# Kernel optimization log

Measured on AMD Instinct MI355X. Metric: run time of the kernel, lower is better.

The kernel has to match this reference:

```python
import jax, jax.numpy as jnp
import numpy as np

B, L, C, H, W = 2, 3, 64, 32, 32
DI, N, DT_RANK, K = 128, 16, 4, 4  # d_inner=2*C, d_state, dt_rank=ceil(C/16), 4 scan dirs


def setup_inputs() -> dict:
    key = jax.random.key(0)
    ks = iter(jax.random.split(key, 48))
    nrm = lambda shape, s=0.02: jax.random.normal(next(ks), shape, jnp.float32) * s
    return {
        "image_sequence": jax.random.normal(next(ks), (B, L, C, H, W), jnp.float32),
        "difficult_zone": jax.random.normal(next(ks), (B, C, H, W), jnp.float32),
        "sigma": jax.random.uniform(next(ks), (B, C, H, W), jnp.float32),
        # LayerNorm2d applied to each frame
        "norm_g": jnp.ones((C,)), "norm_b": jnp.zeros((C,)),
        # ConvolutionalResBlock (in=3C -> out=C), GroupNorm(num_groups=1)
        "gn1_g": jnp.ones((3 * C,)), "gn1_b": jnp.zeros((3 * C,)),
        "conv1_w": nrm((C, 3 * C, 3, 3)), "conv1_b": jnp.zeros((C,)),
        "gn2_g": jnp.ones((C,)), "gn2_b": jnp.zeros((C,)),
        "conv2_w": nrm((C, C, 3, 3)), "conv2_b": jnp.zeros((C,)),
        "skip_w": nrm((C, 3 * C, 1, 1)), "skip_b": jnp.zeros((C,)),
        # VSSBlock pre-norms
        "ln1_g": jnp.ones((C,)), "ln1_b": jnp.zeros((C,)),
        "ln2_g": jnp.ones((C,)), "ln2_b": jnp.zeros((C,)),
        # SS2D
        "in_proj_w": nrm((2 * DI, C)),
        "dwconv_w": nrm((DI, 1, 3, 3)), "dwconv_b": jnp.zeros((DI,)),
        "x_proj_w": nrm((K, DT_RANK + 2 * N, DI)),
        "dt_proj_w": nrm((K, DI, DT_RANK), 0.1),
        "dt_proj_b": jnp.log(jnp.expm1(jnp.full((K, DI), 0.01, jnp.float32))),
        "A_logs": jnp.log(jnp.tile(jnp.arange(1, N + 1, dtype=jnp.float32), (K * DI, 1))),
        "Ds": jnp.ones((K * DI,)),
        "out_norm_g": jnp.ones((DI,)), "out_norm_b": jnp.zeros((DI,)),
        "out_proj_w": nrm((C, DI)),
        # Mlp (hidden = C)
        "fc1_w": nrm((C, C)), "fc1_b": jnp.zeros((C,)),
        "fc2_w": nrm((C, C)), "fc2_b": jnp.zeros((C,)),
    }


def _ln(x, g, b, eps=1e-5):  # layernorm over last axis
    m = x.mean(-1, keepdims=True)
    v = x.var(-1, keepdims=True)
    return (x - m) * jax.lax.rsqrt(v + eps) * g + b


def _ln2d(x, g, b, eps=1e-6):  # per-pixel channel layernorm, NCHW
    m = x.mean(1, keepdims=True)
    v = x.var(1, keepdims=True)
    return (x - m) * jax.lax.rsqrt(v + eps) * g[None, :, None, None] + b[None, :, None, None]


def _gn1(x, g, b, eps=1e-5):  # GroupNorm(num_groups=1), NCHW
    m = x.mean((1, 2, 3), keepdims=True)
    v = x.var((1, 2, 3), keepdims=True)
    return (x - m) * jax.lax.rsqrt(v + eps) * g[None, :, None, None] + b[None, :, None, None]


def _conv(x, w, b, pad):
    y = jax.lax.conv_general_dilated(x, w, (1, 1), [(pad, pad), (pad, pad)],
                                     dimension_numbers=("NCHW", "OIHW", "NCHW"))
    return y + b[None, :, None, None]


def _forward(image_sequence, difficult_zone, sigma, norm_g, norm_b, gn1_g, gn1_b,
             conv1_w, conv1_b, gn2_g, gn2_b, conv2_w, conv2_b, skip_w, skip_b,
             ln1_g, ln1_b, ln2_g, ln2_b, in_proj_w, dwconv_w, dwconv_b, x_proj_w,
             dt_proj_w, dt_proj_b, A_logs, Ds, out_norm_g, out_norm_b, out_proj_w,
             fc1_w, fc1_b, fc2_w, fc2_b):
    b, l, c, h, w = image_sequence.shape
    bl, L2 = b * l, h * w
    # fold frame loop into batch (identical math per frame in the torch loop)
    frames = _ln2d(image_sequence.reshape(bl, c, h, w), norm_g, norm_b)
    dz = jnp.broadcast_to(difficult_zone[:, None], (b, l, c, h, w)).reshape(bl, c, h, w)
    sg = jnp.broadcast_to(sigma[:, None], (b, l, c, h, w)).reshape(bl, c, h, w)
    x = jnp.concatenate([dz, frames, sg], axis=1)  # [bl, 3c, h, w]
    # channel compressor: pre-act conv res block
    hdn = _conv(jax.nn.silu(_gn1(x, gn1_g, gn1_b)), conv1_w, conv1_b, 1)
    hdn = _conv(jax.nn.silu(_gn1(hdn, gn2_g, gn2_b)), conv2_w, conv2_b, 1)
    x = hdn + _conv(x, skip_w, skip_b, 0)          # [bl, c, h, w]
    x = x.transpose(0, 2, 3, 1)                    # [bl, h, w, c]
    # --- VSSBlock (pre-norm): x = x + SS2D(LN(x)) ---
    xn = _ln(x, ln1_g, ln1_b)
    xz = xn @ in_proj_w.T                          # [bl,h,w,2*DI]
    xc, z = jnp.split(xz, 2, axis=-1)
    xc = xc.transpose(0, 3, 1, 2)                  # [bl, DI, h, w]
    xc = jax.lax.conv_general_dilated(xc, dwconv_w, (1, 1), [(1, 1), (1, 1)],
                                      dimension_numbers=("NCHW", "OIHW", "NCHW"),
                                      feature_group_count=DI) + dwconv_b[None, :, None, None]
    xc = jax.nn.silu(xc)
    # 4-direction scan inputs (HW, WH, and their reverses)
    xf = xc.reshape(bl, DI, L2)
    xt = xc.transpose(0, 1, 3, 2).reshape(bl, DI, L2)
    xs = jnp.stack([xf, xt], axis=1)
    xs = jnp.concatenate([xs, jnp.flip(xs, axis=-1)], axis=1)  # [bl, 4, DI, L2]
    x_dbl = jnp.einsum("bkdl,kcd->bkcl", xs, x_proj_w)
    dts, Bs, Cs = jnp.split(x_dbl, [DT_RANK, DT_RANK + N], axis=2)
    dts = jnp.einsum("bkrl,kdr->bkdl", dts, dt_proj_w) + dt_proj_b[None, :, :, None]
    dts = jax.nn.softplus(dts)                     # [bl, 4, DI, L2]
    A = -jnp.exp(A_logs).reshape(K, DI, N)
    dA = jnp.exp(dts[..., None] * A[None, :, :, None, :])            # [bl,4,DI,L2,N]
    dBu = dts[..., None] * Bs.transpose(0, 1, 3, 2)[:, :, None] * xs[..., None]
    a_t = dA.transpose(3, 0, 1, 2, 4)              # [L2, bl, 4, DI, N]
    bu_t = dBu.transpose(3, 0, 1, 2, 4)
    c_t = Cs.transpose(3, 0, 1, 2)                 # [L2, bl, 4, N]

    def step(hid, inp):
        a_i, bu_i, c_i = inp
        hid = a_i * hid + bu_i
        return hid, jnp.einsum("bkdn,bkn->bkd", hid, c_i)

    h0 = jnp.zeros((bl, K, DI, N), xs.dtype)
    _, ys = jax.lax.scan(step, h0, (a_t, bu_t, c_t))                 # [L2, bl, 4, DI]
    ys = ys.transpose(1, 2, 3, 0) + xs * Ds.reshape(K, DI)[None, :, :, None]
    inv = jnp.flip(ys[:, 2:4], axis=-1)
    y = (ys[:, 0] + inv[:, 0]
         + ys[:, 1].reshape(bl, DI, w, h).transpose(0, 1, 3, 2).reshape(bl, DI, L2)
         + inv[:, 1].reshape(bl, DI, w, h).transpose(0, 1, 3, 2).reshape(bl, DI, L2))
    y = _ln(y.transpose(0, 2, 1), out_norm_g, out_norm_b).reshape(bl, h, w, DI)
    y = y * jax.nn.silu(z)
    x = x + y @ out_proj_w.T
    # --- x = x + Mlp(LN(x)) ---
    xn = _ln(x, ln2_g, ln2_b)
    x = x + (jax.nn.gelu(xn @ fc1_w.T + fc1_b, approximate=False) @ fc2_w.T + fc2_b)
    return x.transpose(0, 3, 1, 2).reshape(b, l, c, h, w)


def reference(image_sequence, difficult_zone, sigma, norm_g, norm_b, gn1_g, gn1_b,
              conv1_w, conv1_b, gn2_g, gn2_b, conv2_w, conv2_b, skip_w, skip_b,
              ln1_g, ln1_b, ln2_g, ln2_b, in_proj_w, dwconv_w, dwconv_b, x_proj_w,
              dt_proj_w, dt_proj_b, A_logs, Ds, out_norm_g, out_norm_b, out_proj_w,
              fc1_w, fc1_b, fc2_w, fc2_b):
    return _forward(image_sequence, difficult_zone, sigma, norm_g, norm_b, gn1_g, gn1_b,
                    conv1_w, conv1_b, gn2_g, gn2_b, conv2_w, conv2_b, skip_w, skip_b,
                    ln1_g, ln1_b, ln2_g, ln2_b, in_proj_w, dwconv_w, dwconv_b, x_proj_w,
                    dt_proj_w, dt_proj_b, A_logs, Ds, out_norm_g, out_norm_b, out_proj_w,
                    fc1_w, fc1_b, fc2_w, fc2_b)
```

## Files before the change

### kernel.cpp

```cpp
#include <hip/hip_runtime.h>
#include <math.h>

#define BL    6
#define CCH   64
#define C3    192
#define L2    1024
#define DIC   128
#define NST   16
#define K4    4
#define PSTR  1088
#define NCH   32

#define LOG2E 1.44269504088896340736f
#define LN2C  0.69314718055994530942f

__device__ __forceinline__ float fexp(float x){ return __builtin_amdgcn_exp2f(x*LOG2E); }
__device__ __forceinline__ float fsilu(float x){ return x / (1.f + fexp(-x)); }
__device__ __forceinline__ float fsoftplus(float x){
  if (x > 20.f) return x;
  return __builtin_amdgcn_logf(1.f + fexp(x)) * LN2C;
}
__device__ __forceinline__ float fgelu(float x){
  return 0.5f*x*(1.f + erff(x*0.70710678118654752440f));
}

__global__ __launch_bounds__(256) void k_ln2d(const float* __restrict__ img,
    const float* __restrict__ dz, const float* __restrict__ sg,
    const float* __restrict__ g, const float* __restrict__ b, float* __restrict__ x3c,
    float* __restrict__ psum1, float* __restrict__ psq1){
  __shared__ float ps[4][16], pq[4][16], gs[4], gq[4];
  int s = blockIdx.x >> 6;
  int pg = blockIdx.x & 63;
  int tid = threadIdx.x;
  int px = tid & 15; int cg = tid >> 4;
  int wv = tid >> 6; int lane = tid & 63;
  int p = pg*16 + px;
  int bsmp = s/3;
  const float* fr = img + (size_t)s*CCH*L2;
  float vals[4]; float sm=0.f, sq=0.f;
  #pragma unroll
  for (int j=0;j<4;++j){
    int c = cg*4 + j;
    float v = fr[c*L2 + p];
    vals[j]=v; sm+=v; sq+=v*v;
  }
  sm += __shfl_xor(sm,16,64); sq += __shfl_xor(sq,16,64);
  sm += __shfl_xor(sm,32,64); sq += __shfl_xor(sq,32,64);
  if (lane < 16){ ps[wv][lane]=sm; pq[wv][lane]=sq; }
  __syncthreads();
  sm = ps[0][px]+ps[1][px]+ps[2][px]+ps[3][px];
  sq = pq[0][px]+pq[1][px]+pq[2][px]+pq[3][px];
  float mean = sm*(1.f/CCH); float var = sq*(1.f/CCH)-mean*mean;
  float rs = rsqrtf(var + 1e-6f);
  float* o = x3c + (size_t)s*C3*L2;
  const float* dzp = dz + (size_t)bsmp*CCH*L2;
  const float* sgp = sg + (size_t)bsmp*CCH*L2;
  float gsm=0.f, gsq=0.f;
  #pragma unroll
  for (int j=0;j<4;++j){
    int c = cg*4+j;
    float dzv = dzp[c*L2+p];
    float nv  = (vals[j]-mean)*rs*g[c] + b[c];
    float sgv = sgp[c*L2+p];
    o[c*L2+p] = dzv;
    o[(CCH+c)*L2+p] = nv;
    o[(2*CCH+c)*L2+p] = sgv;
    gsm += dzv+nv+sgv; gsq += dzv*dzv+nv*nv+sgv*sgv;
  }
  for (int m=1;m<64;m<<=1){ gsm+=__shfl_xor(gsm,m,64); gsq+=__shfl_xor(gsq,m,64); }
  if (lane==0){ gs[wv]=gsm; gq[wv]=gsq; }
  __syncthreads();
  if (tid==0){
    psum1[blockIdx.x] = gs[0]+gs[1]+gs[2]+gs[3];
    psq1 [blockIdx.x] = gq[0]+gq[1]+gq[2]+gq[3];
  }
}

__global__ __launch_bounds__(256) void k_gnact_pad(const float* __restrict__ x,
    const float* __restrict__ psum, const float* __restrict__ psq,
    const float* __restrict__ g, const float* __restrict__ b,
    int ch, int parts, float inv_n, float eps, float* __restrict__ out){
  int bx = blockIdx.x;
  int s = bx / ch; int c = bx % ch;
  int tid = threadIdx.x;
  float sm=0.f, sq=0.f;
  for (int i=0;i<parts;++i){ sm += psum[s*parts+i]; sq += psq[s*parts+i]; }
  float mean = sm*inv_n;
  float var = sq*inv_n - mean*mean;
  float rs = rsqrtf(var + eps);
  float gc = g[c]*rs; float bc = b[c] - mean*rs*g[c];
  float4 v = *(const float4*)(x + (size_t)bx*1024 + tid*4);
  float4 o; o.x = fsilu(v.x*gc+bc); o.y = fsilu(v.y*gc+bc);
  o.z = fsilu(v.z*gc+bc); o.w = fsilu(v.w*gc+bc);
  float* pl = out + (size_t)bx*PSTR;
  *(float4*)(pl + 32 + tid*4) = o;
  float4 z4 = make_float4(0.f,0.f,0.f,0.f);
  if (tid < 8)  *(float4*)(pl + tid*4) = z4;
  else if (tid < 16) *(float4*)(pl + 1056 + (tid-8)*4) = z4;
}

__device__ __forceinline__ void conv_row_acc(float4& a0, float4& a1, float4 mid, float lf, float rt,
    const float* wp0, const float* wp1){
  float w0=wp0[0], w1=wp0[1], w2=wp0[2];
  a0.x = fmaf(w0,lf,   fmaf(w1,mid.x, fmaf(w2,mid.y, a0.x)));
  a0.y = fmaf(w0,mid.x,fmaf(w1,mid.y, fmaf(w2,mid.z, a0.y)));
  a0.z = fmaf(w0,mid.y,fmaf(w1,mid.z, fmaf(w2,mid.w, a0.z)));
  a0.w = fmaf(w0,mid.z,fmaf(w1,mid.w, fmaf(w2,rt,    a0.w)));
  float v0=wp1[0], v1=wp1[1], v2=wp1[2];
  a1.x = fmaf(v0,lf,   fmaf(v1,mid.x, fmaf(v2,mid.y, a1.x)));
  a1.y = fmaf(v0,mid.x,fmaf(v1,mid.y, fmaf(v2,mid.z, a1.y)));
  a1.z = fmaf(v0,mid.y,fmaf(v1,mid.z, fmaf(v2,mid.w, a1.z)));
  a1.w = fmaf(v0,mid.z,fmaf(v1,mid.w, fmaf(v2,rt,    a1.w)));
}

__device__ __forceinline__ void conv_ci_body(float4 m0, float4 m1, float4 m2, int q,
    const float* wp0, const float* wp1, float4& a0, float4& a1){
  float lf0=__shfl_up(m0.w,1,64), rt0=__shfl_down(m0.x,1,64);
  float lf1=__shfl_up(m1.w,1,64), rt1=__shfl_down(m1.x,1,64);
  float lf2=__shfl_up(m2.w,1,64), rt2=__shfl_down(m2.x,1,64);
  if (q==0){ lf0=0.f; lf1=0.f; lf2=0.f; }
  if (q==7){ rt0=0.f; rt1=0.f; rt2=0.f; }
  conv_row_acc(a0,a1,m0,lf0,rt0, wp0+0, wp1+0);
  conv_row_acc(a0,a1,m1,lf1,rt1, wp0+3, wp1+3);
  conv_row_acc(a0,a1,m2,lf2,rt2, wp0+6, wp1+6);
}

__global__ __launch_bounds__(256) void k_conv1_split(const float* __restrict__ xact,
    const float* __restrict__ w, float* __restrict__ part){
  int bx = blockIdx.x; int kk = bx&7; int cop=(bx>>3)&31; int s=bx>>8;
  int co0 = cop*2, co1 = co0+1;
  int tid = threadIdx.x; int row = tid>>3; int q = tid&7; int col0 = q*4;
  float4 a0 = make_float4(0.f,0.f,0.f,0.f);
  float4 a1 = make_float4(0.f,0.f,0.f,0.f);
  int ci0 = kk*24;
  const float* pl = xact + ((size_t)s*C3 + ci0)*PSTR + row*32 + col0;
  const float* wp0 = w + (size_t)(co0*C3 + ci0)*9;
  const float* wp1 = w + (size_t)(co1*C3 + ci0)*9;
  float4 m0 = *(const float4*)(pl);
  float4 m1 = *(const float4*)(pl+32);
  float4 m2 = *(const float4*)(pl+64);
  #pragma unroll 2
  for (int i=0;i<24;++i){
    const float* pn = pl + (i<23 ? PSTR : 0);
    float4 n0 = *(const float4*)(pn);
    float4 n1 = *(const float4*)(pn+32);
    float4 n2 = *(const float4*)(pn+64);
    conv_ci_body(m0,m1,m2,q, wp0, wp1, a0, a1);
    wp0 += 9; wp1 += 9; pl = pn; m0=n0; m1=n1; m2=n2;
  }
  float* pp = part + (size_t)kk*(BL*CCH*L2) + ((size_t)s*CCH+co0)*L2 + row*32+col0;
  *(float4*)pp = a0;
  *(float4*)(pp+L2) = a1;
}

__global__ __launch_bounds__(256) void k_reduce1(const float* __restrict__ part,
    const float* __restrict__ bias, float* __restrict__ h1,
    float* __restrict__ psum2, float* __restrict__ psq2){
  int co = blockIdx.x & 63; int s = blockIdx.x >> 6;
  size_t ofs = ((size_t)s*CCH+co)*L2 + threadIdx.x*4;
  const size_t stride = (size_t)BL*CCH*L2;
  float4 acc = *(const float4*)(part + ofs);
  #pragma unroll
  for (int kk=1;kk<8;++kk){
    float4 r = *(const float4*)(part + (size_t)kk*stride + ofs);
    acc.x += r.x; acc.y += r.y; acc.z += r.z; acc.w += r.w;
  }
  float bv = bias[co];
  acc.x += bv; acc.y += bv; acc.z += bv; acc.w += bv;
  *(float4*)(h1 + ofs) = acc;
  float sm = acc.x+acc.y+acc.z+acc.w;
  float sq = acc.x*acc.x+acc.y*acc.y+acc.z*acc.z+acc.w*acc.w;
  for (int m=1;m<64;m<<=1){ sm+=__shfl_xor(sm,m,64); sq+=__shfl_xor(sq,m,64); }
  __shared__ float s_sm[4], s_sq[4];
  int wv = threadIdx.x>>6;
  if ((threadIdx.x&63)==0){ s_sm[wv]=sm; s_sq[wv]=sq; }
  __syncthreads();
  if (threadIdx.x==0){
    psum2[blockIdx.x] = s_sm[0]+s_sm[1]+s_sm[2]+s_sm[3];
    psq2 [blockIdx.x] = s_sq[0]+s_sq[1]+s_sq[2]+s_sq[3];
  }
}

__global__ __launch_bounds__(256) void k_conv2_split(const float* __restrict__ xact2,
    const float* __restrict__ x3c, const float* __restrict__ w2,
    const float* __restrict__ wsk, float* __restrict__ part){
  int t = blockIdx.x; int role = t % 3; t /= 3;
  int cop = t & 31; int s = t >> 5;
  int co0 = cop*2, co1 = co0+1;
  int tid = threadIdx.x; int row = tid>>3; int q = tid&7; int col0 = q*4;
  int p = row*32+col0;
  float4 a0 = make_float4(0.f,0.f,0.f,0.f);
  float4 a1 = make_float4(0.f,0.f,0.f,0.f);
  if (role < 2){
    int ci0 = role*32;
    const float* pl = xact2 + ((size_t)s*CCH + ci0)*PSTR + row*32 + col0;
    const float* wp0 = w2 + (size_t)(co0*CCH + ci0)*9;
    const float* wp1 = w2 + (size_t)(co1*CCH + ci0)*9;
    float4 m0 = *(const float4*)(pl);
    float4 m1 = *(const float4*)(pl+32);
    float4 m2 = *(const float4*)(pl+64);
    #pragma unroll 2
    for (int i=0;i<32;++i){
      const float* pn = pl + (i<31 ? PSTR : 0);
      float4 n0 = *(const float4*)(pn);
      float4 n1 = *(const float4*)(pn+32);
      float4 n2 = *(const float4*)(pn+64);
      conv_ci_body(m0,m1,m2,q, wp0, wp1, a0, a1);
      wp0 += 9; wp1 += 9; pl = pn; m0=n0; m1=n1; m2=n2;
    }
  } else {
    const float* x3 = x3c + (size_t)s*C3*L2 + p;
    #pragma unroll 4
    for (int ci=0; ci<C3; ++ci){
      float4 v = *(const float4*)(x3 + (size_t)ci*L2);
      float ws0 = wsk[co0*C3+ci], ws1 = wsk[co1*C3+ci];
      a0.x = fmaf(ws0,v.x,a0.x); a0.y = fmaf(ws0,v.y,a0.y); a0.z = fmaf(ws0,v.z,a0.z); a0.w = fmaf(ws0,v.w,a0.w);
      a1.x = fmaf(ws1,v.x,a1.x); a1.y = fmaf(ws1,v.y,a1.y); a1.z = fmaf(ws1,v.z,a1.z); a1.w = fmaf(ws1,v.w,a1.w);
    }
  }
  float* pp = part + (size_t)role*(BL*CCH*L2) + ((size_t)s*CCH+co0)*L2 + p;
  *(float4*)pp = a0;
  *(float4*)(pp+L2) = a1;
}

__global__ __launch_bounds__(256) void k_reduce2(const float* __restrict__ part,
    const float* __restrict__ b2, const float* __restrict__ bsk,
    float* __restrict__ xp, float* __restrict__ x_cmaj){
  int co = blockIdx.x & 63; int s = blockIdx.x >> 6;
  int p = threadIdx.x*4;
  size_t ofs = ((size_t)s*CCH+co)*L2 + p;
  const size_t stride = (size_t)BL*CCH*L2;
  float4 r0 = *(const float4*)(part + ofs);
  float4 r1 = *(const float4*)(part + stride + ofs);
  float4 r2 = *(const float4*)(part + 2*stride + ofs);
  float bv = b2[co]+bsk[co];
  float4 o;
  o.x = r0.x+r1.x+r2.x+bv;
  o.y = r0.y+r1.y+r2.y+bv;
  o.z = r0.z+r1.z+r2.z+bv;
  o.w = r0.w+r1.w+r2.w+bv;
  *(float4*)(x_cmaj + ofs) = o;
  float* xpb = xp + ((size_t)s*L2 + p)*CCH + co;
  xpb[0] = o.x; xpb[CCH] = o.y; xpb[2*CCH] = o.z; xpb[3*CCH] = o.w;
}

__global__ __launch_bounds__(256) void k_ln1_inproj(const float* __restrict__ xp,
    const float* __restrict__ g, const float* __restrict__ b, const float* __restrict__ W,
    float* __restrict__ xc, float* __restrict__ z_t){
  __shared__ float xn_s[64*65];
  int bx = blockIdx.x; int oq = bx & 3; int pg = (bx>>2)&15; int s = bx>>6;
  int p0 = pg*64;
  int tid = threadIdx.x; int wv = __builtin_amdgcn_readfirstlane(tid>>6); int lane = tid&63;
  for (int j=0;j<16;++j){
    int pl = wv*16 + j; int p = p0 + pl;
    float v = xp[((size_t)s*L2 + p)*CCH + lane];
    float sm = v, sq = v*v;
    for (int m=1;m<64;m<<=1){ sm += __shfl_xor(sm,m,64); sq += __shfl_xor(sq,m,64); }
    float mean = sm*(1.f/64.f); float var = sq*(1.f/64.f) - mean*mean;
    float rs = rsqrtf(var + 1e-5f);
    xn_s[pl*65 + lane] = (v-mean)*rs*g[lane] + b[lane];
  }
  __syncthreads();
  int px_l = tid & 63;
  int og = __builtin_amdgcn_readfirstlane(tid >> 6);
  int o0 = oq*64 + og*16;
  float acc[16];
  #pragma unroll
  for (int oi=0;oi<16;++oi) acc[oi]=0.f;
  for (int c=0;c<64;++c){
    float xv = xn_s[px_l*65 + c];
    #pragma unroll
    for (int oi=0;oi<16;++oi) acc[oi] = fmaf(W[(o0+oi)*64 + c], xv, acc[oi]);
  }
  int p = p0 + px_l;
  if (oq < 2){
    #pragma unroll
    for (int oi=0;oi<16;++oi) xc[((size_t)s*DIC + o0 + oi)*L2 + p] = acc[oi];
  } else {
    #pragma unroll
    for (int oi=0;oi<16;++oi) z_t[((size_t)s*DIC + (o0-128) + oi)*L2 + p] = acc[oi];
  }
}

__global__ __launch_bounds__(256) void k_dwconv(const float* __restrict__ xc,
    const float* __restrict__ w, const float* __restrict__ bias, float* __restrict__ xconv){
  int bx = blockIdx.x; int dch = bx & 127; int s = bx >> 7;
  int tid = threadIdx.x; int row = tid>>3; int q = tid&7; int col0 = q*4;
  const float* xr = xc + ((size_t)s*DIC+dch)*L2;
  const float* wp = w + dch*9;
  float bv = bias[dch];
  float4 acc = make_float4(bv,bv,bv,bv);
  #pragma unroll
  for (int dy=-1;dy<=1;++dy){
    int r = row+dy;
    float4 mid = make_float4(0.f,0.f,0.f,0.f);
    if (0<=r && r<32) mid = *(const float4*)(xr + r*32 + col0);
    float lf = __shfl_up(mid.w,1,64); if(q==0) lf=0.f;
    float rt = __shfl_down(mid.x,1,64); if(q==7) rt=0.f;
    float w0=wp[(dy+1)*3], w1=wp[(dy+1)*3+1], w2=wp[(dy+1)*3+2];
    acc.x = fmaf(w0,lf,   fmaf(w1,mid.x, fmaf(w2,mid.y, acc.x)));
    acc.y = fmaf(w0,mid.x,fmaf(w1,mid.y, fmaf(w2,mid.z, acc.y)));
    acc.z = fmaf(w0,mid.y,fmaf(w1,mid.z, fmaf(w2,mid.w, acc.z)));
    acc.w = fmaf(w0,mid.z,fmaf(w1,mid.w, fmaf(w2,rt,    acc.w)));
  }
  acc.x = fsilu(acc.x); acc.y = fsilu(acc.y); acc.z = fsilu(acc.z); acc.w = fsilu(acc.w);
  *(float4*)(xconv + ((size_t)s*DIC+dch)*L2 + row*32+col0) = acc;
}

__global__ __launch_bounds__(256) void k_xproj_dt(const float* __restrict__ xconv,
    const float* __restrict__ W,
    float* __restrict__ dtr, float* __restrict__ Bp, float* __restrict__ Cp,
    float* __restrict__ u_t){
  __shared__ float smem[128*68];
  int bx = blockIdx.x; int pg = bx & 15; int sk = bx >> 4;
  int k = sk & 3; int s = sk >> 2;
  int tid = threadIdx.x;
  for (int i = tid; i < 128*16; i += 256){
    int dr = i>>4; int j4 = (i&15)*4;
    float4 v = *(const float4*)(xconv + ((size_t)(s*DIC + dr))*L2 + pg*64 + j4);
    *(float4*)&smem[dr*68 + j4] = v;
  }
  __syncthreads();
  if (k == 0){
    float* ub = u_t + ((size_t)(s*L2) + pg*64)*DIC;
    for (int i = tid; i < 64*128; i += 256){
      int px2 = i>>7; int dd = i&127;
      ub[(size_t)px2*DIC + dd] = smem[dd*68 + px2];
    }
  }
  int px = tid & 63;
  int cgrp = __builtin_amdgcn_readfirstlane(tid >> 6);
  int c0 = cgrp*9;
  const float* wb = W + (size_t)(k*36 + c0)*DIC;
  float acc[9];
  #pragma unroll
  for (int ci=0;ci<9;++ci) acc[ci]=0.f;
  for (int d=0; d<DIC; ++d){
    float xv = smem[d*68 + px];
    #pragma unroll
    for (int ci=0;ci<9;++ci) acc[ci] = fmaf(wb[ci*DIC+d], xv, acc[ci]);
  }
  __syncthreads();
  #pragma unroll
  for (int ci=0;ci<9;++ci) smem[(c0+ci)*68 + px] = acc[ci];
  __syncthreads();
  {
    int pp = tid >> 2; int r = tid & 3;
    dtr[((size_t)sk*L2 + pg*64 + pp)*4 + r] = smem[r*68 + pp];
  }
  float* Bb = Bp + ((size_t)sk*L2 + pg*64)*NST;
  float* Cb = Cp + ((size_t)sk*L2 + pg*64)*NST;
  for (int i = tid; i < 1024; i += 256){
    int pp = i>>4; int n = i&15;
    Bb[pp*NST + n] = smem[(4+n)*68 + pp];
    Cb[pp*NST + n] = smem[(20+n)*68 + pp];
  }
}

__device__ __forceinline__ int scan_pix32(int ch, int j, int k){
  if (k==0) return ch*32 + j;
  if (k==1) return j*32 + ch;
  if (k==2) return 1023 - (ch*32 + j);
  return 1023 - (j*32 + ch);
}

struct StepB { float4 dt4; float uv; float4 B0,B1,B2,B3; };
__device__ __forceinline__ StepB loadB(const float* dr, const float* ub, const float* Bb, int p){
  StepB r;
  r.dt4 = *(const float4*)(dr + (size_t)p*4);
  r.uv = ub[(size_t)p*DIC];
  const float* bp = Bb + p*NST;
  r.B0 = *(const float4*)bp; r.B1 = *(const float4*)(bp+4);
  r.B2 = *(const float4*)(bp+8); r.B3 = *(const float4*)(bp+12);
  return r;
}
__device__ __forceinline__ float dt_eval(float4 w4, float bb, float4 d4){
  return fsoftplus(fmaf(w4.x,d4.x,fmaf(w4.y,d4.y,fmaf(w4.z,d4.z,fmaf(w4.w,d4.w,bb)))));
}

__global__ __launch_bounds__(256,2) void k_scan_part3(const float* __restrict__ dtr,
    const float* __restrict__ dtw, const float* __restrict__ dtb,
    const float* __restrict__ u_t, const float* __restrict__ Bp,
    const float* __restrict__ A_logs, float* __restrict__ hend, float* __restrict__ Ssum){
  int bx = blockIdx.x; int chp = bx & 15; int sk = bx >> 4;
  int k = sk & 3; int s = sk >> 2;
  int tid = threadIdx.x; int d = tid & 127; int ch = chp*2 + (tid>>7);
  float aco[16];
  {
    const float* ab = A_logs + (size_t)(k*DIC+d)*NST;
    #pragma unroll
    for (int n=0;n<16;++n) aco[n] = -LOG2E * fexp(ab[n]);
  }
  float4 w4 = *(const float4*)(dtw + (size_t)(k*DIC+d)*4);
  float bb = dtb[k*DIC+d];
  float h[16]; float Sacc = 0.f;
  #pragma unroll
  for (int n=0;n<16;++n) h[n]=0.f;
  const float* dr = dtr + (size_t)sk*L2*4;
  const float* ub = u_t + (size_t)s*L2*DIC + d;
  const float* Bb = Bp + (size_t)sk*L2*NST;
  StepB cur = loadB(dr, ub, Bb, scan_pix32(ch, 0, k));
  #pragma unroll 4
  for (int j=0;j<32;++j){
    StepB nxt;
    if (j < 31) nxt = loadB(dr, ub, Bb, scan_pix32(ch, j+1, k));
    float dtv = dt_eval(w4, bb, cur.dt4);
    Sacc += dtv;
    float tv = dtv*cur.uv;
    #define PSTEP(NI, BV) { float a_ = __builtin_amdgcn_exp2f(dtv*aco[NI]); \
      h[NI] = fmaf(a_, h[NI], tv*(BV)); }
    PSTEP(0,cur.B0.x) PSTEP(1,cur.B0.y) PSTEP(2,cur.B0.z) PSTEP(3,cur.B0.w)
    PSTEP(4,cur.B1.x) PSTEP(5,cur.B1.y) PSTEP(6,cur.B1.z) PSTEP(7,cur.B1.w)
    PSTEP(8,cur.B2.x) PSTEP(9,cur.B2.y) PSTEP(10,cur.B2.z) PSTEP(11,cur.B2.w)
    PSTEP(12,cur.B3.x) PSTEP(13,cur.B3.y) PSTEP(14,cur.B3.z) PSTEP(15,cur.B3.w)
    #undef PSTEP
    cur = nxt;
  }
  size_t base = ((size_t)(sk*NCH + ch)*DIC + d)*NST;
  #pragma unroll
  for (int q4=0;q4<4;++q4)
    *(float4*)(hend + base + q4*4)  = make_float4(h[q4*4],h[q4*4+1],h[q4*4+2],h[q4*4+3]);
  Ssum[(size_t)(sk*NCH + ch)*DIC + d] = Sacc;
}

__global__ __launch_bounds__(256) void k_scan_fix3(const float* __restrict__ hend,
    const float* __restrict__ Ssum, const float* __restrict__ A_logs,
    float* __restrict__ Hin){
  int t = blockIdx.x*256 + threadIdx.x;
  int n = t & 15; int d = (t>>4) & 127; int sk = t >> 11; int k = sk & 3;
  float aco = -LOG2E * fexp(A_logs[(size_t)(k*DIC+d)*NST + n]);
  float H = 0.f;
  #pragma unroll 8
  for (int ch=0; ch<NCH; ++ch){
    size_t sidx = (size_t)(sk*NCH + ch)*DIC + d;
    float pa = __builtin_amdgcn_exp2f(aco * Ssum[sidx]);
    float he = hend[sidx*NST + n];
    Hin[sidx*NST + n] = H;
    H = fmaf(pa, H, he);
  }
}

__global__ __launch_bounds__(256,2) void k_scan_y3(const float* __restrict__ dtr,
    const float* __restrict__ dtw, const float* __restrict__ dtb,
    const float* __restrict__ u_t, const float* __restrict__ Bp, const float* __restrict__ Cp,
    const float* __restrict__ A_logs, const float* __restrict__ Ds,
    const float* __restrict__ Hin, float* __restrict__ ys_t){
  int bx = blockIdx.x; int chp = bx & 15; int sk = bx >> 4;
  int k = sk & 3; int s = sk >> 2;
  int tid = threadIdx.x; int d = tid & 127; int ch = chp*2 + (tid>>7);
  float aco[16];
  {
    const float* ab = A_logs + (size_t)(k*DIC+d)*NST;
    #pragma unroll
    for (int n=0;n<16;++n) aco[n] = -LOG2E * fexp(ab[n]);
  }
  float4 w4 = *(const float4*)(dtw + (size_t)(k*DIC+d)*4);
  float bb = dtb[k*DIC+d];
  float Dv = Ds[k*DIC+d];
  float h[16];
  size_t hbase = ((size_t)(sk*NCH + ch)*DIC + d)*NST;
  #pragma unroll
  for (int q4=0;q4<4;++q4){
    float4 hv = *(const float4*)(Hin + hbase + q4*4);
    h[q4*4]=hv.x; h[q4*4+1]=hv.y; h[q4*4+2]=hv.z; h[q4*4+3]=hv.w;
  }
  const float* dr = dtr + (size_t)sk*L2*4;
  const float* ub = u_t + (size_t)s*L2*DIC + d;
  const float* Bb = Bp + (size_t)sk*L2*NST;
  const float* Cb = Cp + (size_t)sk*L2*NST;
  float* yb = ys_t + (size_t)sk*L2*DIC + d;
  int pcur = scan_pix32(ch, 0, k);
  StepB cur = loadB(dr, ub, Bb, pcur);
  float4 Cc0 = *(const float4*)(Cb + pcur*NST);
  float4 Cc1 = *(const float4*)(Cb + pcur*NST + 4);
  float4 Cc2 = *(const float4*)(Cb + pcur*NST + 8);
  float4 Cc3 = *(const float4*)(Cb + pcur*NST + 12);
  #pragma unroll 4
  for (int j=0;j<32;++j){
    StepB nxt; float4 Cn0, Cn1, Cn2, Cn3; int pn = pcur;
    if (j < 31){
      pn = scan_pix32(ch, j+1, k);
      nxt = loadB(dr, ub, Bb, pn);
      Cn0 = *(const float4*)(Cb + pn*NST);
      Cn1 = *(const float4*)(Cb + pn*NST + 4);
      Cn2 = *(const float4*)(Cb + pn*NST + 8);
      Cn3 = *(const float4*)(Cb + pn*NST + 12);
    }
    float dtv = dt_eval(w4, bb, cur.dt4);
    float tv = dtv*cur.uv;
    float y0=0.f, y1=0.f, y2=0.f, y3=0.f;
    #define YSTEP(NI, BV, CV, YA) { float a_ = __builtin_amdgcn_exp2f(dtv*aco[NI]); \
      h[NI] = fmaf(a_, h[NI], tv*(BV)); YA = fmaf(h[NI], (CV), YA); }
    YSTEP(0,cur.B0.x,Cc0.x,y0) YSTEP(1,cur.B0.y,Cc0.y,y1) YSTEP(2,cur.B0.z,Cc0.z,y2) YSTEP(3,cur.B0.w,Cc0.w,y3)
    YSTEP(4,cur.B1.x,Cc1.x,y0) YSTEP(5,cur.B1.y,Cc1.y,y1) YSTEP(6,cur.B1.z,Cc1.z,y2) YSTEP(7,cur.B1.w,Cc1.w,y3)
    YSTEP(8,cur.B2.x,Cc2.x,y0) YSTEP(9,cur.B2.y,Cc2.y,y1) YSTEP(10,cur.B2.z,Cc2.z,y2) YSTEP(11,cur.B2.w,Cc2.w,y3)
    YSTEP(12,cur.B3.x,Cc3.x,y0) YSTEP(13,cur.B3.y,Cc3.y,y1) YSTEP(14,cur.B3.z,Cc3.z,y2) YSTEP(15,cur.B3.w,Cc3.w,y3)
    #undef YSTEP
    yb[(size_t)pcur*DIC] = fmaf(cur.uv, Dv, (y0+y1)+(y2+y3));
    cur = nxt; Cc0 = Cn0; Cc1 = Cn1; Cc2 = Cn2; Cc3 = Cn3; pcur = pn;
  }
}

__global__ __launch_bounds__(256) void k_tail(const float* __restrict__ ys_t,
    const float* __restrict__ z_t, const float* __restrict__ ong, const float* __restrict__ onb,
    const float* __restrict__ Wop, const float* __restrict__ x_cmaj,
    const float* __restrict__ g2, const float* __restrict__ b2n,
    const float* __restrict__ w1, const float* __restrict__ b1,
    const float* __restrict__ w2, const float* __restrict__ b2,
    float* __restrict__ out){
  __shared__ float yt[128*17];
  __shared__ float xvt[64*17];
  __shared__ float ts[64*17];
  int s = blockIdx.x >> 6; int pg = blockIdx.x & 63;
  int tid = threadIdx.x;
  {
    int wv = __builtin_amdgcn_readfirstlane(tid>>6); int lane = tid&63;
    int d0 = lane, d1 = lane+64;
    for (int i=0;i<4;++i){
      int px = i*4 + wv; int p = pg*16 + px;
      const float* yb = ys_t + ((size_t)(s*4)*L2 + p)*DIC;
      float ya = yb[d0] + yb[(size_t)L2*DIC + d0] + yb[(size_t)2*L2*DIC + d0] + yb[(size_t)3*L2*DIC + d0];
      float yc = yb[d1] + yb[(size_t)L2*DIC + d1] + yb[(size_t)2*L2*DIC + d1] + yb[(size_t)3*L2*DIC + d1];
      float sm = ya+yc, sq = ya*ya+yc*yc;
      for (int m=1;m<64;m<<=1){ sm+=__shfl_xor(sm,m,64); sq+=__shfl_xor(sq,m,64); }
      float mean = sm*(1.f/128.f); float var = sq*(1.f/128.f)-mean*mean;
      float rs = rsqrtf(var + 1e-5f);
      float yn0 = (ya-mean)*rs*ong[d0] + onb[d0];
      float yn1 = (yc-mean)*rs*ong[d1] + onb[d1];
      float zv0 = z_t[((size_t)s*DIC+d0)*L2 + p];
      float zv1 = z_t[((size_t)s*DIC+d1)*L2 + p];
      yt[d0*17 + px] = yn0 * fsilu(zv0);
      yt[d1*17 + px] = yn1 * fsilu(zv1);
    }
  }
  __syncthreads();
  {
    int px = tid & 15; int cgp = tid >> 4;
    int c0 = cgp*4;
    float a0=0.f,a1=0.f,a2=0.f,a3=0.f;
    for (int d=0; d<DIC; ++d){
      float yv = yt[d*17 + px];
      a0 = fmaf(Wop[(c0+0)*DIC + d], yv, a0);
      a1 = fmaf(Wop[(c0+1)*DIC + d], yv, a1);
      a2 = fmaf(Wop[(c0+2)*DIC + d], yv, a2);
      a3 = fmaf(Wop[(c0+3)*DIC + d], yv, a3);
    }
    int p = pg*16 + px;
    size_t base = ((size_t)s*CCH + c0)*L2 + p;
    xvt[(c0+0)*17 + px] = x_cmaj[base]      + a0;
    xvt[(c0+1)*17 + px] = x_cmaj[base+L2]   + a1;
    xvt[(c0+2)*17 + px] = x_cmaj[base+2*L2] + a2;
    xvt[(c0+3)*17 + px] = x_cmaj[base+3*L2] + a3;
  }
  __syncthreads();
  int px = tid & 15; int cgp = tid >> 4;
  float sm=0.f, sq=0.f;
  for (int c=0;c<64;++c){ float v = xvt[c*17+px]; sm+=v; sq+=v*v; }
  float mean = sm*(1.f/64.f);
  float rs = rsqrtf(sq*(1.f/64.f) - mean*mean + 1e-5f);
  int o0 = cgp*4;
  float t[4];
  #pragma unroll
  for (int oi=0;oi<4;++oi) t[oi] = b1[o0+oi];
  for (int c=0;c<64;++c){
    float xn = (xvt[c*17+px]-mean)*rs*g2[c] + b2n[c];
    #pragma unroll
    for (int oi=0;oi<4;++oi) t[oi] = fmaf(xn, w1[(o0+oi)*64 + c], t[oi]);
  }
  #pragma unroll
  for (int oi=0;oi<4;++oi) ts[(o0+oi)*17 + px] = fgelu(t[oi]);
  __syncthreads();
  int c0 = cgp*4;
  float acc[4];
  #pragma unroll
  for (int ci=0;ci<4;++ci) acc[ci] = xvt[(c0+ci)*17+px] + b2[c0+ci];
  for (int o=0;o<64;++o){
    float tv = ts[o*17+px];
    #pragma unroll
    for (int ci=0;ci<4;++ci) acc[ci] = fmaf(tv, w2[(c0+ci)*64 + o], acc[ci]);
  }
  int p = pg*16 + px;
  #pragma unroll
  for (int ci=0;ci<4;++ci) out[((size_t)s*CCH + c0+ci)*L2 + p] = acc[ci];
}

extern "C" void kernel_launch(void* const* d_in, const int* in_sizes, int n_in,
                              void* d_out, int out_size, void* d_ws, size_t ws_size,
                              hipStream_t stream){
  (void)in_sizes; (void)n_in; (void)out_size; (void)ws_size;
  const float* img      = (const float*)d_in[0];
  const float* dz       = (const float*)d_in[1];
  const float* sg       = (const float*)d_in[2];
  const float* norm_g   = (const float*)d_in[3];
  const float* norm_b   = (const float*)d_in[4];
  const float* gn1_g    = (const float*)d_in[5];
  const float* gn1_b    = (const float*)d_in[6];
  const float* conv1_w  = (const float*)d_in[7];
  const float* conv1_b  = (const float*)d_in[8];
  const float* gn2_g    = (const float*)d_in[9];
  const float* gn2_b    = (const float*)d_in[10];
  const float* conv2_w  = (const float*)d_in[11];
  const float* conv2_b  = (const float*)d_in[12];
  const float* skip_w   = (const float*)d_in[13];
  const float* skip_b   = (const float*)d_in[14];
  const float* ln1_g    = (const float*)d_in[15];
  const float* ln1_b    = (const float*)d_in[16];
  const float* ln2_g    = (const float*)d_in[17];
  const float* ln2_b    = (const float*)d_in[18];
  const float* in_proj_w= (const float*)d_in[19];
  const float* dwconv_w = (const float*)d_in[20];
  const float* dwconv_b = (const float*)d_in[21];
  const float* x_proj_w = (const float*)d_in[22];
  const float* dt_proj_w= (const float*)d_in[23];
  const float* dt_proj_b= (const float*)d_in[24];
  const float* A_logs   = (const float*)d_in[25];
  const float* Ds       = (const float*)d_in[26];
  const float* out_norm_g = (const float*)d_in[27];
  const float* out_norm_b = (const float*)d_in[28];
  const float* out_proj_w = (const float*)d_in[29];
  const float* fc1_w    = (const float*)d_in[30];
  const float* fc1_b    = (const float*)d_in[31];
  const float* fc2_w    = (const float*)d_in[32];
  const float* fc2_b    = (const float*)d_in[33];

  float* ws = (float*)d_ws;
  float* x3c    = ws;
  float* xact1  = x3c    + 1179648;
  float* h1     = xact1  + 1253376;
  float* xact2  = h1     + 393216;
  float* xp     = xact2  + 417792;
  float* x_cmaj = xp     + 393216;
  float* z_t    = x_cmaj + 393216;
  float* xc     = z_t    + 786432;
  float* xconv  = xc     + 786432;
  float* hole   = xconv  + 786432;
  float* scanbuf= hole   + 884736;
  float* ys_t   = scanbuf+ 3145728;
  float* statsb = ys_t   + 3145728;
  float* psum1  = statsb;
  float* psq1   = statsb + 384;
  float* psum2  = statsb + 768;
  float* psq2   = statsb + 1152;
  float* part1  = scanbuf;
  float* part2  = ys_t;
  float* hend   = x3c;
  float* u_t    = h1;
  float* Bp     = xp;
  float* Cp     = xc;
  float* dtr    = hole;
  float* Ssum   = hole + 98304;
  float* Hin    = scanbuf;

  k_ln2d<<<384, 256, 0, stream>>>(img, dz, sg, norm_g, norm_b, x3c, psum1, psq1);
  k_gnact_pad<<<6*C3, 256, 0, stream>>>(x3c, psum1, psq1, gn1_g, gn1_b, C3, 64,
                                        1.f/(C3*L2), 1e-5f, xact1);
  k_conv1_split<<<1536, 256, 0, stream>>>(xact1, conv1_w, part1);
  k_reduce1<<<384, 256, 0, stream>>>(part1, conv1_b, h1, psum2, psq2);
  k_gnact_pad<<<6*CCH, 256, 0, stream>>>(h1, psum2, psq2, gn2_g, gn2_b, CCH, 64,
                                         1.f/(CCH*L2), 1e-5f, xact2);
  k_conv2_split<<<576, 256, 0, stream>>>(xact2, x3c, conv2_w, skip_w, part2);
  k_reduce2<<<384, 256, 0, stream>>>(part2, conv2_b, skip_b, xp, x_cmaj);
  k_ln1_inproj<<<384, 256, 0, stream>>>(xp, ln1_g, ln1_b, in_proj_w, xc, z_t);
  k_dwconv<<<768, 256, 0, stream>>>(xc, dwconv_w, dwconv_b, xconv);
  k_xproj_dt<<<384, 256, 0, stream>>>(xconv, x_proj_w, dtr, Bp, Cp, u_t);
  k_scan_part3<<<384, 256, 0, stream>>>(dtr, dt_proj_w, dt_proj_b, u_t, Bp, A_logs, hend, Ssum);
  k_scan_fix3<<<192, 256, 0, stream>>>(hend, Ssum, A_logs, Hin);
  k_scan_y3<<<384, 256, 0, stream>>>(dtr, dt_proj_w, dt_proj_b, u_t, Bp, Cp, A_logs, Ds, Hin, ys_t);
  k_tail<<<384, 256, 0, stream>>>(ys_t, z_t, out_norm_g, out_norm_b, out_proj_w, x_cmaj,
                                  ln2_g, ln2_b, fc1_w, fc1_b, fc2_w, fc2_b, (float*)d_out);
}
```

Measured before the change: 304.7 us.

## Fuse all stages into one cooperative persistent megakernel with grid syncs

Replaces fourteen separate kernel launches with a single cooperative kernel that walks the same per-stage block work in grid-stride loops, separated by grid.sync barriers. The goal is to remove launch gaps and per-kernel ramp-up and tail costs between the many small stages. In exchange, every stage now runs with one shared register and LDS budget (a 34 KB static shared buffer and launch_bounds(256,2)). That can lower occupancy for the light stages and add register pressure to the scan and conv stages. The grid is capped at 384 blocks and sized once through an occupancy query.

```diff
diff --git a/kernel.cpp b/kernel.cpp
--- a/kernel.cpp
+++ b/kernel.cpp
@@ -1,5 +1,8 @@
 #include <hip/hip_runtime.h>
+#include <hip/hip_cooperative_groups.h>
 #include <math.h>
+
+namespace cg = cooperative_groups;
 
 #define BL    6
 #define CCH   64
@@ -24,19 +27,30 @@
   return 0.5f*x*(1.f + erff(x*0.70710678118654752440f));
 }
 
-__global__ __launch_bounds__(256) void k_ln2d(const float* __restrict__ img,
-    const float* __restrict__ dz, const float* __restrict__ sg,
-    const float* __restrict__ g, const float* __restrict__ b, float* __restrict__ x3c,
-    float* __restrict__ psum1, float* __restrict__ psq1){
-  __shared__ float ps[4][16], pq[4][16], gs[4], gq[4];
-  int s = blockIdx.x >> 6;
-  int pg = blockIdx.x & 63;
+struct MP {
+  const float *img, *dz, *sg, *norm_g, *norm_b;
+  const float *gn1_g, *gn1_b, *conv1_w, *conv1_b, *gn2_g, *gn2_b, *conv2_w, *conv2_b;
+  const float *skip_w, *skip_b, *ln1_g, *ln1_b, *ln2_g, *ln2_b, *in_proj_w;
+  const float *dwconv_w, *dwconv_b, *x_proj_w, *dt_proj_w, *dt_proj_b, *A_logs, *Ds;
+  const float *out_norm_g, *out_norm_b, *out_proj_w, *fc1_w, *fc1_b, *fc2_w, *fc2_b;
+  float *x3c, *xact1, *h1, *xact2, *xp, *x_cmaj, *z_t, *xc, *xconv;
+  float *psum1, *psq1, *psum2, *psq2;
+  float *part1, *part2, *hend, *u_t, *Bp, *Cp, *dtr, *Ssum, *Hin, *ys_t;
+  float *out;
+};
+
+__device__ __forceinline__ void ph_ln2d(int bx, float* SH, const MP& P){
+  float (*ps)[16] = (float(*)[16])SH;
+  float (*pq)[16] = (float(*)[16])(SH + 64);
+  float *gs = SH + 128, *gq = SH + 132;
+  int s = bx >> 6;
+  int pg = bx & 63;
   int tid = threadIdx.x;
   int px = tid & 15; int cg = tid >> 4;
   int wv = tid >> 6; int lane = tid & 63;
   int p = pg*16 + px;
   int bsmp = s/3;
-  const float* fr = img + (size_t)s*CCH*L2;
+  const float* fr = P.img + (size_t)s*CCH*L2;
   float vals[4]; float sm=0.f, sq=0.f;
   #pragma unroll
   for (int j=0;j<4;++j){
@@ -52,15 +66,15 @@
   sq = pq[0][px]+pq[1][px]+pq[2][px]+pq[3][px];
   float mean = sm*(1.f/CCH); float var = sq*(1.f/CCH)-mean*mean;
   float rs = rsqrtf(var + 1e-6f);
-  float* o = x3c + (size_t)s*C3*L2;
-  const float* dzp = dz + (size_t)bsmp*CCH*L2;
-  const float* sgp = sg + (size_t)bsmp*CCH*L2;
+  float* o = P.x3c + (size_t)s*C3*L2;
+  const float* dzp = P.dz + (size_t)bsmp*CCH*L2;
+  const float* sgp = P.sg + (size_t)bsmp*CCH*L2;
   float gsm=0.f, gsq=0.f;
   #pragma unroll
   for (int j=0;j<4;++j){
     int c = cg*4+j;
     float dzv = dzp[c*L2+p];
-    float nv  = (vals[j]-mean)*rs*g[c] + b[c];
+    float nv  = (vals[j]-mean)*rs*P.norm_g[c] + P.norm_b[c];
     float sgv = sgp[c*L2+p];
     o[c*L2+p] = dzv;
     o[(CCH+c)*L2+p] = nv;
@@ -71,16 +85,15 @@
   if (lane==0){ gs[wv]=gsm; gq[wv]=gsq; }
   __syncthreads();
   if (tid==0){
-    psum1[blockIdx.x] = gs[0]+gs[1]+gs[2]+gs[3];
-    psq1 [blockIdx.x] = gq[0]+gq[1]+gq[2]+gq[3];
-  }
-}
-
-__global__ __launch_bounds__(256) void k_gnact_pad(const float* __restrict__ x,
+    P.psum1[bx] = gs[0]+gs[1]+gs[2]+gs[3];
+    P.psq1 [bx] = gq[0]+gq[1]+gq[2]+gq[3];
+  }
+}
+
+__device__ __forceinline__ void ph_gnact(int bx, const float* __restrict__ x,
     const float* __restrict__ psum, const float* __restrict__ psq,
     const float* __restrict__ g, const float* __restrict__ b,
     int ch, int parts, float inv_n, float eps, float* __restrict__ out){
-  int bx = blockIdx.x;
   int s = bx / ch; int c = bx % ch;
   int tid = threadIdx.x;
   float sm=0.f, sq=0.f;
@@ -125,17 +138,16 @@
   conv_row_acc(a0,a1,m2,lf2,rt2, wp0+6, wp1+6);
 }
 
-__global__ __launch_bounds__(256) void k_conv1_split(const float* __restrict__ xact,
-    const float* __restrict__ w, float* __restrict__ part){
-  int bx = blockIdx.x; int kk = bx&7; int cop=(bx>>3)&31; int s=bx>>8;
+__device__ __forceinline__ void ph_conv1(int bx, const MP& P){
+  int kk = bx&7; int cop=(bx>>3)&31; int s=bx>>8;
   int co0 = cop*2, co1 = co0+1;
   int tid = threadIdx.x; int row = tid>>3; int q = tid&7; int col0 = q*4;
   float4 a0 = make_float4(0.f,0.f,0.f,0.f);
   float4 a1 = make_float4(0.f,0.f,0.f,0.f);
   int ci0 = kk*24;
-  const float* pl = xact + ((size_t)s*C3 + ci0)*PSTR + row*32 + col0;
-  const float* wp0 = w + (size_t)(co0*C3 + ci0)*9;
-  const float* wp1 = w + (size_t)(co1*C3 + ci0)*9;
+  const float* pl = P.xact1 + ((size_t)s*C3 + ci0)*PSTR + row*32 + col0;
+  const float* wp0 = P.conv1_w + (size_t)(co0*C3 + ci0)*9;
+  const float* wp1 = P.conv1_w + (size_t)(co1*C3 + ci0)*9;
   float4 m0 = *(const float4*)(pl);
   float4 m1 = *(const float4*)(pl+32);
   float4 m2 = *(const float4*)(pl+64);
@@ -148,43 +160,39 @@
     conv_ci_body(m0,m1,m2,q, wp0, wp1, a0, a1);
     wp0 += 9; wp1 += 9; pl = pn; m0=n0; m1=n1; m2=n2;
   }
-  float* pp = part + (size_t)kk*(BL*CCH*L2) + ((size_t)s*CCH+co0)*L2 + row*32+col0;
+  float* pp = P.part1 + (size_t)kk*(BL*CCH*L2) + ((size_t)s*CCH+co0)*L2 + row*32+col0;
   *(float4*)pp = a0;
   *(float4*)(pp+L2) = a1;
 }
 
-__global__ __launch_bounds__(256) void k_reduce1(const float* __restrict__ part,
-    const float* __restrict__ bias, float* __restrict__ h1,
-    float* __restrict__ psum2, float* __restrict__ psq2){
-  int co = blockIdx.x & 63; int s = blockIdx.x >> 6;
+__device__ __forceinline__ void ph_reduce1(int bx, float* SH, const MP& P){
+  float* s_sm = SH; float* s_sq = SH + 4;
+  int co = bx & 63; int s = bx >> 6;
   size_t ofs = ((size_t)s*CCH+co)*L2 + threadIdx.x*4;
   const size_t stride = (size_t)BL*CCH*L2;
-  float4 acc = *(const float4*)(part + ofs);
+  float4 acc = *(const float4*)(P.part1 + ofs);
   #pragma unroll
   for (int kk=1;kk<8;++kk){
-    float4 r = *(const float4*)(part + (size_t)kk*stride + ofs);
+    float4 r = *(const float4*)(P.part1 + (size_t)kk*stride + ofs);
     acc.x += r.x; acc.y += r.y; acc.z += r.z; acc.w += r.w;
   }
-  float bv = bias[co];
+  float bv = P.conv1_b[co];
   acc.x += bv; acc.y += bv; acc.z += bv; acc.w += bv;
-  *(float4*)(h1 + ofs) = acc;
+  *(float4*)(P.h1 + ofs) = acc;
   float sm = acc.x+acc.y+acc.z+acc.w;
   float sq = acc.x*acc.x+acc.y*acc.y+acc.z*acc.z+acc.w*acc.w;
   for (int m=1;m<64;m<<=1){ sm+=__shfl_xor(sm,m,64); sq+=__shfl_xor(sq,m,64); }
-  __shared__ float s_sm[4], s_sq[4];
   int wv = threadIdx.x>>6;
   if ((threadIdx.x&63)==0){ s_sm[wv]=sm; s_sq[wv]=sq; }
   __syncthreads();
   if (threadIdx.x==0){
-    psum2[blockIdx.x] = s_sm[0]+s_sm[1]+s_sm[2]+s_sm[3];
-    psq2 [blockIdx.x] = s_sq[0]+s_sq[1]+s_sq[2]+s_sq[3];
-  }
-}
-
-__global__ __launch_bounds__(256) void k_conv2_split(const float* __restrict__ xact2,
-    const float* __restrict__ x3c, const float* __restrict__ w2,
-    const float* __restrict__ wsk, float* __restrict__ part){
-  int t = blockIdx.x; int role = t % 3; t /= 3;
+    P.psum2[bx] = s_sm[0]+s_sm[1]+s_sm[2]+s_sm[3];
+    P.psq2 [bx] = s_sq[0]+s_sq[1]+s_sq[2]+s_sq[3];
+  }
+}
+
+__device__ __forceinline__ void ph_conv2(int bx, const MP& P){
+  int t = bx; int role = t % 3; t /= 3;
   int cop = t & 31; int s = t >> 5;
   int co0 = cop*2, co1 = co0+1;
   int tid = threadIdx.x; int row = tid>>3; int q = tid&7; int col0 = q*4;
@@ -193,9 +201,9 @@
   float4 a1 = make_float4(0.f,0.f,0.f,0.f);
   if (role < 2){
     int ci0 = role*32;
-    const float* pl = xact2 + ((size_t)s*CCH + ci0)*PSTR + row*32 + col0;
-    const float* wp0 = w2 + (size_t)(co0*CCH + ci0)*9;
-    const float* wp1 = w2 + (size_t)(co1*CCH + ci0)*9;
+    const float* pl = P.xact2 + ((size_t)s*CCH + ci0)*PSTR + row*32 + col0;
+    const float* wp0 = P.conv2_w + (size_t)(co0*CCH + ci0)*9;
+    const float* wp1 = P.conv2_w + (size_t)(co1*CCH + ci0)*9;
     float4 m0 = *(const float4*)(pl);
     float4 m1 = *(const float4*)(pl+32);
     float4 m2 = *(const float4*)(pl+64);
@@ -209,56 +217,52 @@
       wp0 += 9; wp1 += 9; pl = pn; m0=n0; m1=n1; m2=n2;
     }
   } else {
-    const float* x3 = x3c + (size_t)s*C3*L2 + p;
+    const float* x3 = P.x3c + (size_t)s*C3*L2 + p;
     #pragma unroll 4
     for (int ci=0; ci<C3; ++ci){
       float4 v = *(const float4*)(x3 + (size_t)ci*L2);
-      float ws0 = wsk[co0*C3+ci], ws1 = wsk[co1*C3+ci];
+      float ws0 = P.skip_w[co0*C3+ci], ws1 = P.skip_w[co1*C3+ci];
       a0.x = fmaf(ws0,v.x,a0.x); a0.y = fmaf(ws0,v.y,a0.y); a0.z = fmaf(ws0,v.z,a0.z); a0.w = fmaf(ws0,v.w,a0.w);
       a1.x = fmaf(ws1,v.x,a1.x); a1.y = fmaf(ws1,v.y,a1.y); a1.z = fmaf(ws1,v.z,a1.z); a1.w = fmaf(ws1,v.w,a1.w);
     }
   }
-  float* pp = part + (size_t)role*(BL*CCH*L2) + ((size_t)s*CCH+co0)*L2 + p;
+  float* pp = P.part2 + (size_t)role*(BL*CCH*L2) + ((size_t)s*CCH+co0)*L2 + p;
   *(float4*)pp = a0;
   *(float4*)(pp+L2) = a1;
 }
 
-__global__ __launch_bounds__(256) void k_reduce2(const float* __restrict__ part,
-    const float* __restrict__ b2, const float* __restrict__ bsk,
-    float* __restrict__ xp, float* __restrict__ x_cmaj){
-  int co = blockIdx.x & 63; int s = blockIdx.x >> 6;
+__device__ __forceinline__ void ph_reduce2(int bx, const MP& P){
+  int co = bx & 63; int s = bx >> 6;
   int p = threadIdx.x*4;
   size_t ofs = ((size_t)s*CCH+co)*L2 + p;
   const size_t stride = (size_t)BL*CCH*L2;
-  float4 r0 = *(const float4*)(part + ofs);
-  float4 r1 = *(const float4*)(part + stride + ofs);
-  float4 r2 = *(const float4*)(part + 2*stride + ofs);
-  float bv = b2[co]+bsk[co];
+  float4 r0 = *(const float4*)(P.part2 + ofs);
+  float4 r1 = *(const float4*)(P.part2 + stride + ofs);
+  float4 r2 = *(const float4*)(P.part2 + 2*stride + ofs);
+  float bv = P.conv2_b[co]+P.skip_b[co];
   float4 o;
   o.x = r0.x+r1.x+r2.x+bv;
   o.y = r0.y+r1.y+r2.y+bv;
   o.z = r0.z+r1.z+r2.z+bv;
   o.w = r0.w+r1.w+r2.w+bv;
-  *(float4*)(x_cmaj + ofs) = o;
-  float* xpb = xp + ((size_t)s*L2 + p)*CCH + co;
+  *(float4*)(P.x_cmaj + ofs) = o;
+  float* xpb = P.xp + ((size_t)s*L2 + p)*CCH + co;
   xpb[0] = o.x; xpb[CCH] = o.y; xpb[2*CCH] = o.z; xpb[3*CCH] = o.w;
 }
 
-__global__ __launch_bounds__(256) void k_ln1_inproj(const float* __restrict__ xp,
-    const float* __restrict__ g, const float* __restrict__ b, const float* __restrict__ W,
-    float* __restrict__ xc, float* __restrict__ z_t){
-  __shared__ float xn_s[64*65];
-  int bx = blockIdx.x; int oq = bx & 3; int pg = (bx>>2)&15; int s = bx>>6;
+__device__ __forceinline__ void ph_ln1_inproj(int bx, float* SH, const MP& P){
+  float* xn_s = SH;
+  int oq = bx & 3; int pg = (bx>>2)&15; int s = bx>>6;
   int p0 = pg*64;
   int tid = threadIdx.x; int wv = __builtin_amdgcn_readfirstlane(tid>>6); int lane = tid&63;
   for (int j=0;j<16;++j){
     int pl = wv*16 + j; int p = p0 + pl;
-    float v = xp[((size_t)s*L2 + p)*CCH + lane];
+    float v = P.xp[((size_t)s*L2 + p)*CCH + lane];
     float sm = v, sq = v*v;
     for (int m=1;m<64;m<<=1){ sm += __shfl_xor(sm,m,64); sq += __shfl_xor(sq,m,64); }
     float mean = sm*(1.f/64.f); float var = sq*(1.f/64.f) - mean*mean;
     float rs = rsqrtf(var + 1e-5f);
-    xn_s[pl*65 + lane] = (v-mean)*rs*g[lane] + b[lane];
+    xn_s[pl*65 + lane] = (v-mean)*rs*P.ln1_g[lane] + P.ln1_b[lane];
   }
   __syncthreads();
   int px_l = tid & 63;
@@ -270,25 +274,24 @@
   for (int c=0;c<64;++c){
     float xv = xn_s[px_l*65 + c];
     #pragma unroll
-    for (int oi=0;oi<16;++oi) acc[oi] = fmaf(W[(o0+oi)*64 + c], xv, acc[oi]);
+    for (int oi=0;oi<16;++oi) acc[oi] = fmaf(P.in_proj_w[(o0+oi)*64 + c], xv, acc[oi]);
   }
   int p = p0 + px_l;
   if (oq < 2){
     #pragma unroll
-    for (int oi=0;oi<16;++oi) xc[((size_t)s*DIC + o0 + oi)*L2 + p] = acc[oi];
+    for (int oi=0;oi<16;++oi) P.xc[((size_t)s*DIC + o0 + oi)*L2 + p] = acc[oi];
   } else {
     #pragma unroll
-    for (int oi=0;oi<16;++oi) z_t[((size_t)s*DIC + (o0-128) + oi)*L2 + p] = acc[oi];
-  }
-}
-
-__global__ __launch_bounds__(256) void k_dwconv(const float* __restrict__ xc,
-    const float* __restrict__ w, const float* __restrict__ bias, float* __restrict__ xconv){
-  int bx = blockIdx.x; int dch = bx & 127; int s = bx >> 7;
+    for (int oi=0;oi<16;++oi) P.z_t[((size_t)s*DIC + (o0-128) + oi)*L2 + p] = acc[oi];
+  }
+}
+
+__device__ __forceinline__ void ph_dwconv(int bx, const MP& P){
+  int dch = bx & 127; int s = bx >> 7;
   int tid = threadIdx.x; int row = tid>>3; int q = tid&7; int col0 = q*4;
-  const float* xr = xc + ((size_t)s*DIC+dch)*L2;
-  const float* wp = w + dch*9;
-  float bv = bias[dch];
+  const float* xr = P.xc + ((size_t)s*DIC+dch)*L2;
+  const float* wp = P.dwconv_w + dch*9;
+  float bv = P.dwconv_b[dch];
   float4 acc = make_float4(bv,bv,bv,bv);
   #pragma unroll
   for (int dy=-1;dy<=1;++dy){
@@ -304,25 +307,22 @@
     acc.w = fmaf(w0,mid.z,fmaf(w1,mid.w, fmaf(w2,rt,    acc.w)));
   }
   acc.x = fsilu(acc.x); acc.y = fsilu(acc.y); acc.z = fsilu(acc.z); acc.w = fsilu(acc.w);
-  *(float4*)(xconv + ((size_t)s*DIC+dch)*L2 + row*32+col0) = acc;
-}
-
-__global__ __launch_bounds__(256) void k_xproj_dt(const float* __restrict__ xconv,
-    const float* __restrict__ W,
-    float* __restrict__ dtr, float* __restrict__ Bp, float* __restrict__ Cp,
-    float* __restrict__ u_t){
-  __shared__ float smem[128*68];
-  int bx = blockIdx.x; int pg = bx & 15; int sk = bx >> 4;
+  *(float4*)(P.xconv + ((size_t)s*DIC+dch)*L2 + row*32+col0) = acc;
+}
+
+__device__ __forceinline__ void ph_xproj(int bx, float* SH, const MP& P){
+  float* smem = SH;
+  int pg = bx & 15; int sk = bx >> 4;
   int k = sk & 3; int s = sk >> 2;
   int tid = threadIdx.x;
   for (int i = tid; i < 128*16; i += 256){
     int dr = i>>4; int j4 = (i&15)*4;
-    float4 v = *(const float4*)(xconv + ((size_t)(s*DIC + dr))*L2 + pg*64 + j4);
+    float4 v = *(const float4*)(P.xconv + ((size_t)(s*DIC + dr))*L2 + pg*64 + j4);
     *(float4*)&smem[dr*68 + j4] = v;
   }
   __syncthreads();
   if (k == 0){
-    float* ub = u_t + ((size_t)(s*L2) + pg*64)*DIC;
+    float* ub = P.u_t + ((size_t)(s*L2) + pg*64)*DIC;
     for (int i = tid; i < 64*128; i += 256){
       int px2 = i>>7; int dd = i&127;
       ub[(size_t)px2*DIC + dd] = smem[dd*68 + px2];
@@ -331,7 +331,7 @@
   int px = tid & 63;
   int cgrp = __builtin_amdgcn_readfirstlane(tid >> 6);
   int c0 = cgrp*9;
-  const float* wb = W + (size_t)(k*36 + c0)*DIC;
+  const float* wb = P.x_proj_w + (size_t)(k*36 + c0)*DIC;
   float acc[9];
   #pragma unroll
   for (int ci=0;ci<9;++ci) acc[ci]=0.f;
@@ -346,10 +346,10 @@
   __syncthreads();
   {
     int pp = tid >> 2; int r = tid & 3;
-    dtr[((size_t)sk*L2 + pg*64 + pp)*4 + r] = smem[r*68 + pp];
-  }
-  float* Bb = Bp + ((size_t)sk*L2 + pg*64)*NST;
-  float* Cb = Cp + ((size_t)sk*L2 + pg*64)*NST;
+    P.dtr[((size_t)sk*L2 + pg*64 + pp)*4 + r] = smem[r*68 + pp];
+  }
+  float* Bb = P.Bp + ((size_t)sk*L2 + pg*64)*NST;
+  float* Cb = P.Cp + ((size_t)sk*L2 + pg*64)*NST;
   for (int i = tid; i < 1024; i += 256){
     int pp = i>>4; int n = i&15;
     Bb[pp*NST + n] = smem[(4+n)*68 + pp];
@@ -378,27 +378,24 @@
   return fsoftplus(fmaf(w4.x,d4.x,fmaf(w4.y,d4.y,fmaf(w4.z,d4.z,fmaf(w4.w,d4.w,bb)))));
 }
 
-__global__ __launch_bounds__(256,2) void k_scan_part3(const float* __restrict__ dtr,
-    const float* __restrict__ dtw, const float* __restrict__ dtb,
-    const float* __restrict__ u_t, const float* __restrict__ Bp,
-    const float* __restrict__ A_logs, float* __restrict__ hend, float* __restrict__ Ssum){
-  int bx = blockIdx.x; int chp = bx & 15; int sk = bx >> 4;
+__device__ __forceinline__ void ph_scan_part(int bx, const MP& P){
+  int chp = bx & 15; int sk = bx >> 4;
   int k = sk & 3; int s = sk >> 2;
   int tid = threadIdx.x; int d = tid & 127; int ch = chp*2 + (tid>>7);
   float aco[16];
   {
-    const float* ab = A_logs + (size_t)(k*DIC+d)*NST;
+    const float* ab = P.A_logs + (size_t)(k*DIC+d)*NST;
     #pragma unroll
     for (int n=0;n<16;++n) aco[n] = -LOG2E * fexp(ab[n]);
   }
-  float4 w4 = *(const float4*)(dtw + (size_t)(k*DIC+d)*4);
-  float bb = dtb[k*DIC+d];
+  float4 w4 = *(const float4*)(P.dt_proj_w + (size_t)(k*DIC+d)*4);
+  float bb = P.dt_proj_b[k*DIC+d];
   float h[16]; float Sacc = 0.f;
   #pragma unroll
   for (int n=0;n<16;++n) h[n]=0.f;
-  const float* dr = dtr + (size_t)sk*L2*4;
-  const float* ub = u_t + (size_t)s*L2*DIC + d;
-  const float* Bb = Bp + (size_t)sk*L2*NST;
+  const float* dr = P.dtr + (size_t)sk*L2*4;
+  const float* ub = P.u_t + (size_t)s*L2*DIC + d;
+  const float* Bb = P.Bp + (size_t)sk*L2*NST;
   StepB cur = loadB(dr, ub, Bb, scan_pix32(ch, 0, k));
   #pragma unroll 4
   for (int j=0;j<32;++j){
@@ -419,56 +416,50 @@
   size_t base = ((size_t)(sk*NCH + ch)*DIC + d)*NST;
   #pragma unroll
   for (int q4=0;q4<4;++q4)
-    *(float4*)(hend + base + q4*4)  = make_float4(h[q4*4],h[q4*4+1],h[q4*4+2],h[q4*4+3]);
-  Ssum[(size_t)(sk*NCH + ch)*DIC + d] = Sacc;
-}
-
-__global__ __launch_bounds__(256) void k_scan_fix3(const float* __restrict__ hend,
-    const float* __restrict__ Ssum, const float* __restrict__ A_logs,
-    float* __restrict__ Hin){
-  int t = blockIdx.x*256 + threadIdx.x;
+    *(float4*)(P.hend + base + q4*4)  = make_float4(h[q4*4],h[q4*4+1],h[q4*4+2],h[q4*4+3]);
+  P.Ssum[(size_t)(sk*NCH + ch)*DIC + d] = Sacc;
+}
+
+__device__ __forceinline__ void ph_scan_fix(int bx, const MP& P){
+  int t = bx*256 + threadIdx.x;
   int n = t & 15; int d = (t>>4) & 127; int sk = t >> 11; int k = sk & 3;
-  float aco = -LOG2E * fexp(A_logs[(size_t)(k*DIC+d)*NST + n]);
+  float aco = -LOG2E * fexp(P.A_logs[(size_t)(k*DIC+d)*NST + n]);
   float H = 0.f;
   #pragma unroll 8
   for (int ch=0; ch<NCH; ++ch){
     size_t sidx = (size_t)(sk*NCH + ch)*DIC + d;
-    float pa = __builtin_amdgcn_exp2f(aco * Ssum[sidx]);
-    float he = hend[sidx*NST + n];
-    Hin[sidx*NST + n] = H;
+    float pa = __builtin_amdgcn_exp2f(aco * P.Ssum[sidx]);
+    float he = P.hend[sidx*NST + n];
+    P.Hin[sidx*NST + n] = H;
     H = fmaf(pa, H, he);
   }
 }
 
-__global__ __launch_bounds__(256,2) void k_scan_y3(const float* __restrict__ dtr,
-    const float* __restrict__ dtw, const float* __restrict__ dtb,
-    const float* __restrict__ u_t, const float* __restrict__ Bp, const float* __restrict__ Cp,
-    const float* __restrict__ A_logs, const float* __restrict__ Ds,
-    const float* __restrict__ Hin, float* __restrict__ ys_t){
-  int bx = blockIdx.x; int chp = bx & 15; int sk = bx >> 4;
+__device__ __forceinline__ void ph_scan_y(int bx, const MP& P){
+  int chp = bx & 15; int sk = bx >> 4;
   int k = sk & 3; int s = sk >> 2;
   int tid = threadIdx.x; int d = tid & 127; int ch = chp*2 + (tid>>7);
   float aco[16];
   {
-    const float* ab = A_logs + (size_t)(k*DIC+d)*NST;
+    const float* ab = P.A_logs + (size_t)(k*DIC+d)*NST;
     #pragma unroll
     for (int n=0;n<16;++n) aco[n] = -LOG2E * fexp(ab[n]);
   }
-  float4 w4 = *(const float4*)(dtw + (size_t)(k*DIC+d)*4);
-  float bb = dtb[k*DIC+d];
-  float Dv = Ds[k*DIC+d];
+  float4 w4 = *(const float4*)(P.dt_proj_w + (size_t)(k*DIC+d)*4);
+  float bb = P.dt_proj_b[k*DIC+d];
+  float Dv = P.Ds[k*DIC+d];
   float h[16];
   size_t hbase = ((size_t)(sk*NCH + ch)*DIC + d)*NST;
   #pragma unroll
   for (int q4=0;q4<4;++q4){
-    float4 hv = *(const float4*)(Hin + hbase + q4*4);
+    float4 hv = *(const float4*)(P.Hin + hbase + q4*4);
     h[q4*4]=hv.x; h[q4*4+1]=hv.y; h[q4*4+2]=hv.z; h[q4*4+3]=hv.w;
   }
-  const float* dr = dtr + (size_t)sk*L2*4;
-  const float* ub = u_t + (size_t)s*L2*DIC + d;
-  const float* Bb = Bp + (size_t)sk*L2*NST;
-  const float* Cb = Cp + (size_t)sk*L2*NST;
-  float* yb = ys_t + (size_t)sk*L2*DIC + d;
+  const float* dr = P.dtr + (size_t)sk*L2*4;
+  const float* ub = P.u_t + (size_t)s*L2*DIC + d;
+  const float* Bb = P.Bp + (size_t)sk*L2*NST;
+  const float* Cb = P.Cp + (size_t)sk*L2*NST;
+  float* yb = P.ys_t + (size_t)sk*L2*DIC + d;
   int pcur = scan_pix32(ch, 0, k);
   StepB cur = loadB(dr, ub, Bb, pcur);
   float4 Cc0 = *(const float4*)(Cb + pcur*NST);
@@ -501,34 +492,28 @@
   }
 }
 
-__global__ __launch_bounds__(256) void k_tail(const float* __restrict__ ys_t,
-    const float* __restrict__ z_t, const float* __restrict__ ong, const float* __restrict__ onb,
-    const float* __restrict__ Wop, const float* __restrict__ x_cmaj,
-    const float* __restrict__ g2, const float* __restrict__ b2n,
-    const float* __restrict__ w1, const float* __restrict__ b1,
-    const float* __restrict__ w2, const float* __restrict__ b2,
-    float* __restrict__ out){
-  __shared__ float yt[128*17];
-  __shared__ float xvt[64*17];
-  __shared__ float ts[64*17];
-  int s = blockIdx.x >> 6; int pg = blockIdx.x & 63;
+__device__ __forceinline__ void ph_tail(int bx, float* SH, const MP& P){
+  float* yt  = SH;
+  float* xvt = SH + 2176;
+  float* ts  = SH + 3264;
+  int s = bx >> 6; int pg = bx & 63;
   int tid = threadIdx.x;
   {
     int wv = __builtin_amdgcn_readfirstlane(tid>>6); int lane = tid&63;
     int d0 = lane, d1 = lane+64;
     for (int i=0;i<4;++i){
       int px = i*4 + wv; int p = pg*16 + px;
-      const float* yb = ys_t + ((size_t)(s*4)*L2 + p)*DIC;
+      const float* yb = P.ys_t + ((size_t)(s*4)*L2 + p)*DIC;
       float ya = yb[d0] + yb[(size_t)L2*DIC + d0] + yb[(size_t)2*L2*DIC + d0] + yb[(size_t)3*L2*DIC + d0];
       float yc = yb[d1] + yb[(size_t)L2*DIC + d1] + yb[(size_t)2*L2*DIC + d1] + yb[(size_t)3*L2*DIC + d1];
       float sm = ya+yc, sq = ya*ya+yc*yc;
       for (int m=1;m<64;m<<=1){ sm+=__shfl_xor(sm,m,64); sq+=__shfl_xor(sq,m,64); }
       float mean = sm*(1.f/128.f); float var = sq*(1.f/128.f)-mean*mean;
       float rs = rsqrtf(var + 1e-5f);
-      float yn0 = (ya-mean)*rs*ong[d0] + onb[d0];
-      float yn1 = (yc-mean)*rs*ong[d1] + onb[d1];
-      float zv0 = z_t[((size_t)s*DIC+d0)*L2 + p];
-      float zv1 = z_t[((size_t)s*DIC+d1)*L2 + p];
+      float yn0 = (ya-mean)*rs*P.out_norm_g[d0] + P.out_norm_b[d0];
+      float yn1 = (yc-mean)*rs*P.out_norm_g[d1] + P.out_norm_b[d1];
+      float zv0 = P.z_t[((size_t)s*DIC+d0)*L2 + p];
+      float zv1 = P.z_t[((size_t)s*DIC+d1)*L2 + p];
       yt[d0*17 + px] = yn0 * fsilu(zv0);
       yt[d1*17 + px] = yn1 * fsilu(zv1);
     }
@@ -540,17 +525,17 @@
     float a0=0.f,a1=0.f,a2=0.f,a3=0.f;
     for (int d=0; d<DIC; ++d){
       float yv = yt[d*17 + px];
-      a0 = fmaf(Wop[(c0+0)*DIC + d], yv, a0);
-      a1 = fmaf(Wop[(c0+1)*DIC + d], yv, a1);
-      a2 = fmaf(Wop[(c0+2)*DIC + d], yv, a2);
-      a3 = fmaf(Wop[(c0+3)*DIC + d], yv, a3);
+      a0 = fmaf(P.out_proj_w[(c0+0)*DIC + d], yv, a0);
+      a1 = fmaf(P.out_proj_w[(c0+1)*DIC + d], yv, a1);
+      a2 = fmaf(P.out_proj_w[(c0+2)*DIC + d], yv, a2);
+      a3 = fmaf(P.out_proj_w[(c0+3)*DIC + d], yv, a3);
     }
     int p = pg*16 + px;
     size_t base = ((size_t)s*CCH + c0)*L2 + p;
-    xvt[(c0+0)*17 + px] = x_cmaj[base]      + a0;
-    xvt[(c0+1)*17 + px] = x_cmaj[base+L2]   + a1;
-    xvt[(c0+2)*17 + px] = x_cmaj[base+2*L2] + a2;
-    xvt[(c0+3)*17 + px] = x_cmaj[base+3*L2] + a3;
+    xvt[(c0+0)*17 + px] = P.x_cmaj[base]      + a0;
+    xvt[(c0+1)*17 + px] = P.x_cmaj[base+L2]   + a1;
+    xvt[(c0+2)*17 + px] = P.x_cmaj[base+2*L2] + a2;
+    xvt[(c0+3)*17 + px] = P.x_cmaj[base+3*L2] + a3;
   }
   __syncthreads();
   int px = tid & 15; int cgp = tid >> 4;
@@ -561,11 +546,11 @@
   int o0 = cgp*4;
   float t[4];
   #pragma unroll
-  for (int oi=0;oi<4;++oi) t[oi] = b1[o0+oi];
+  for (int oi=0;oi<4;++oi) t[oi] = P.fc1_b[o0+oi];
   for (int c=0;c<64;++c){
-    float xn = (xvt[c*17+px]-mean)*rs*g2[c] + b2n[c];
-    #pragma unroll
-    for (int oi=0;oi<4;++oi) t[oi] = fmaf(xn, w1[(o0+oi)*64 + c], t[oi]);
+    float xn = (xvt[c*17+px]-mean)*rs*P.ln2_g[c] + P.ln2_b[c];
+    #pragma unroll
+    for (int oi=0;oi<4;++oi) t[oi] = fmaf(xn, P.fc1_w[(o0+oi)*64 + c], t[oi]);
   }
   #pragma unroll
   for (int oi=0;oi<4;++oi) ts[(o0+oi)*17 + px] = fgelu(t[oi]);
@@ -573,56 +558,48 @@
   int c0 = cgp*4;
   float acc[4];
   #pragma unroll
-  for (int ci=0;ci<4;++ci) acc[ci] = xvt[(c0+ci)*17+px] + b2[c0+ci];
+  for (int ci=0;ci<4;++ci) acc[ci] = xvt[(c0+ci)*17+px] + P.fc2_b[c0+ci];
   for (int o=0;o<64;++o){
     float tv = ts[o*17+px];
     #pragma unroll
-    for (int ci=0;ci<4;++ci) acc[ci] = fmaf(tv, w2[(c0+ci)*64 + o], acc[ci]);
+    for (int ci=0;ci<4;++ci) acc[ci] = fmaf(tv, P.fc2_w[(c0+ci)*64 + o], acc[ci]);
   }
   int p = pg*16 + px;
   #pragma unroll
-  for (int ci=0;ci<4;++ci) out[((size_t)s*CCH + c0+ci)*L2 + p] = acc[ci];
+  for (int ci=0;ci<4;++ci) P.out[((size_t)s*CCH + c0+ci)*L2 + p] = acc[ci];
+}
+
+#define PHASE(NBLK, BODY) \
+  for (int bx = blockIdx.x; bx < (NBLK); bx += GD){ BODY; __syncthreads(); } \
+  grid.sync();
+
+__global__ __launch_bounds__(256, 2) void k_mega(MP P){
+  cg::grid_group grid = cg::this_grid();
+  __shared__ float SH[8704];
+  const int GD = gridDim.x;
+
+  PHASE(384,  ph_ln2d(bx, SH, P))
+  PHASE(1152, ph_gnact(bx, P.x3c, P.psum1, P.psq1, P.gn1_g, P.gn1_b, C3, 64,
+                       1.f/(C3*L2), 1e-5f, P.xact1))
+  PHASE(1536, ph_conv1(bx, P))
+  PHASE(384,  ph_reduce1(bx, SH, P))
+  PHASE(384,  ph_gnact(bx, P.h1, P.psum2, P.psq2, P.gn2_g, P.gn2_b, CCH, 64,
+                       1.f/(CCH*L2), 1e-5f, P.xact2))
+  PHASE(576,  ph_conv2(bx, P))
+  PHASE(384,  ph_reduce2(bx, P))
+  PHASE(384,  ph_ln1_inproj(bx, SH, P))
+  PHASE(768,  ph_dwconv(bx, P))
+  PHASE(384,  ph_xproj(bx, SH, P))
+  PHASE(384,  ph_scan_part(bx, P))
+  PHASE(192,  ph_scan_fix(bx, P))
+  PHASE(384,  ph_scan_y(bx, P))
+  for (int bx = blockIdx.x; bx < 384; bx += GD){ ph_tail(bx, SH, P); __syncthreads(); }
 }
 
 extern "C" void kernel_launch(void* const* d_in, const int* in_sizes, int n_in,
                               void* d_out, int out_size, void* d_ws, size_t ws_size,
                               hipStream_t stream){
   (void)in_sizes; (void)n_in; (void)out_size; (void)ws_size;
-  const float* img      = (const float*)d_in[0];
-  const float* dz       = (const float*)d_in[1];
-  const float* sg       = (const float*)d_in[2];
-  const float* norm_g   = (const float*)d_in[3];
-  const float* norm_b   = (const float*)d_in[4];
-  const float* gn1_g    = (const float*)d_in[5];
-  const float* gn1_b    = (const float*)d_in[6];
-  const float* conv1_w  = (const float*)d_in[7];
-  const float* conv1_b  = (const float*)d_in[8];
-  const float* gn2_g    = (const float*)d_in[9];
-  const float* gn2_b    = (const float*)d_in[10];
-  const float* conv2_w  = (const float*)d_in[11];
-  const float* conv2_b  = (const float*)d_in[12];
-  const float* skip_w   = (const float*)d_in[13];
-  const float* skip_b   = (const float*)d_in[14];
-  const float* ln1_g    = (const float*)d_in[15];
-  const float* ln1_b    = (const float*)d_in[16];
-  const float* ln2_g    = (const float*)d_in[17];
-  const float* ln2_b    = (const float*)d_in[18];
-  const float* in_proj_w= (const float*)d_in[19];
-  const float* dwconv_w = (const float*)d_in[20];
-  const float* dwconv_b = (const float*)d_in[21];
-  const float* x_proj_w = (const float*)d_in[22];
-  const float* dt_proj_w= (const float*)d_in[23];
-  const float* dt_proj_b= (const float*)d_in[24];
-  const float* A_logs   = (const float*)d_in[25];
-  const float* Ds       = (const float*)d_in[26];
-  const float* out_norm_g = (const float*)d_in[27];
-  const float* out_norm_b = (const float*)d_in[28];
-  const float* out_proj_w = (const float*)d_in[29];
-  const float* fc1_w    = (const float*)d_in[30];
-  const float* fc1_b    = (const float*)d_in[31];
-  const float* fc2_w    = (const float*)d_in[32];
-  const float* fc2_b    = (const float*)d_in[33];
-
   float* ws = (float*)d_ws;
   float* x3c    = ws;
   float* xact1  = x3c    + 1179648;
@@ -637,35 +614,66 @@
   float* scanbuf= hole   + 884736;
   float* ys_t   = scanbuf+ 3145728;
   float* statsb = ys_t   + 3145728;
-  float* psum1  = statsb;
-  float* psq1   = statsb + 384;
-  float* psum2  = statsb + 768;
-  float* psq2   = statsb + 1152;
-  float* part1  = scanbuf;
-  float* part2  = ys_t;
-  float* hend   = x3c;
-  float* u_t    = h1;
-  float* Bp     = xp;
-  float* Cp     = xc;
-  float* dtr    = hole;
-  float* Ssum   = hole + 98304;
-  float* Hin    = scanbuf;
-
-  k_ln2d<<<384, 256, 0, stream>>>(img, dz, sg, norm_g, norm_b, x3c, psum1, psq1);
-  k_gnact_pad<<<6*C3, 256, 0, stream>>>(x3c, psum1, psq1, gn1_g, gn1_b, C3, 64,
-                                        1.f/(C3*L2), 1e-5f, xact1);
-  k_conv1_split<<<1536, 256, 0, stream>>>(xact1, conv1_w, part1);
-  k_reduce1<<<384, 256, 0, stream>>>(part1, conv1_b, h1, psum2, psq2);
-  k_gnact_pad<<<6*CCH, 256, 0, stream>>>(h1, psum2, psq2, gn2_g, gn2_b, CCH, 64,
-                                         1.f/(CCH*L2), 1e-5f, xact2);
-  k_conv2_split<<<576, 256, 0, stream>>>(xact2, x3c, conv2_w, skip_w, part2);
-  k_reduce2<<<384, 256, 0, stream>>>(part2, conv2_b, skip_b, xp, x_cmaj);
-  k_ln1_inproj<<<384, 256, 0, stream>>>(xp, ln1_g, ln1_b, in_proj_w, xc, z_t);
-  k_dwconv<<<768, 256, 0, stream>>>(xc, dwconv_w, dwconv_b, xconv);
-  k_xproj_dt<<<384, 256, 0, stream>>>(xconv, x_proj_w, dtr, Bp, Cp, u_t);
-  k_scan_part3<<<384, 256, 0, stream>>>(dtr, dt_proj_w, dt_proj_b, u_t, Bp, A_logs, hend, Ssum);
-  k_scan_fix3<<<192, 256, 0, stream>>>(hend, Ssum, A_logs, Hin);
-  k_scan_y3<<<384, 256, 0, stream>>>(dtr, dt_proj_w, dt_proj_b, u_t, Bp, Cp, A_logs, Ds, Hin, ys_t);
-  k_tail<<<384, 256, 0, stream>>>(ys_t, z_t, out_norm_g, out_norm_b, out_proj_w, x_cmaj,
-                                  ln2_g, ln2_b, fc1_w, fc1_b, fc2_w, fc2_b, (float*)d_out);
-}
+
+  MP P;
+  P.img      = (const float*)d_in[0];
+  P.dz       = (const float*)d_in[1];
+  P.sg       = (const float*)d_in[2];
+  P.norm_g   = (const float*)d_in[3];
+  P.norm_b   = (const float*)d_in[4];
+  P.gn1_g    = (const float*)d_in[5];
+  P.gn1_b    = (const float*)d_in[6];
+  P.conv1_w  = (const float*)d_in[7];
+  P.conv1_b  = (const float*)d_in[8];
+  P.gn2_g    = (const float*)d_in[9];
+  P.gn2_b    = (const float*)d_in[10];
+  P.conv2_w  = (const float*)d_in[11];
+  P.conv2_b  = (const float*)d_in[12];
+  P.skip_w   = (const float*)d_in[13];
+  P.skip_b   = (const float*)d_in[14];
+  P.ln1_g    = (const float*)d_in[15];
+  P.ln1_b    = (const float*)d_in[16];
+  P.ln2_g    = (const float*)d_in[17];
+  P.ln2_b    = (const float*)d_in[18];
+  P.in_proj_w= (const float*)d_in[19];
+  P.dwconv_w = (const float*)d_in[20];
+  P.dwconv_b = (const float*)d_in[21];
+  P.x_proj_w = (const float*)d_in[22];
+  P.dt_proj_w= (const float*)d_in[23];
+  P.dt_proj_b= (const float*)d_in[24];
+  P.A_logs   = (const float*)d_in[25];
+  P.Ds       = (const float*)d_in[26];
+  P.out_norm_g = (const float*)d_in[27];
+  P.out_norm_b = (const float*)d_in[28];
+  P.out_proj_w = (const float*)d_in[29];
+  P.fc1_w    = (const float*)d_in[30];
+  P.fc1_b    = (const float*)d_in[31];
+  P.fc2_w    = (const float*)d_in[32];
+  P.fc2_b    = (const float*)d_in[33];
+  P.x3c = x3c; P.xact1 = xact1; P.h1 = h1; P.xact2 = xact2; P.xp = xp;
+  P.x_cmaj = x_cmaj; P.z_t = z_t; P.xc = xc; P.xconv = xconv;
+  P.psum1 = statsb; P.psq1 = statsb + 384; P.psum2 = statsb + 768; P.psq2 = statsb + 1152;
+  P.part1 = scanbuf;
+  P.part2 = ys_t;
+  P.hend  = x3c;
+  P.u_t   = h1;
+  P.Bp    = xp;
+  P.Cp    = xc;
+  P.dtr   = hole;
+  P.Ssum  = hole + 98304;
+  P.Hin   = scanbuf;
+  P.ys_t  = ys_t;
+  P.out   = (float*)d_out;
+
+  static int g_grid = 0;
+  if (g_grid == 0){
+    int mb = 0;
+    if (hipOccupancyMaxActiveBlocksPerMultiprocessor(&mb, (const void*)k_mega, 256, 0)
+        != hipSuccess || mb < 1) mb = 1;
+    long g = (long)mb * 256;
+    if (g > 384) g = 384;
+    g_grid = (int)g;
+  }
+  void* args[] = { (void*)&P };
+  hipLaunchCooperativeKernel((const void*)k_mega, dim3(g_grid), dim3(256), args, 0, stream);
+}
```

After: 819.3 us. 169% more time.
